# Kernel tuning notes

Measured on AMD Instinct MI355X. Metric: run time of the kernel, lower is better.

The kernel has to match this reference:

```python
import jax, jax.numpy as jnp
import numpy as np

N_NODES = 100000
N_EDGES = 800000
B = 4000            # number of pair subgraphs
GNN_IN = 428        # embed_dim(300) + 128 structural features
H = 64              # GIN hidden_channels
HID = 512           # PATH_DIM
EMB = 300           # numberbatch embedding dim
NUM_CLS = 151       # VG object classes
N_LAYERS = 3


def setup_inputs() -> dict:
    key = jax.random.key(0)
    ks = jax.random.split(key, 32)
    inp = {
        "pred_pairs": jax.random.randint(ks[0], (B, 2), 0, NUM_CLS, dtype=jnp.int32),
        "x": jax.random.normal(ks[1], (N_NODES, GNN_IN), dtype=jnp.float32),
        "edge_index": jax.random.randint(ks[2], (2, N_EDGES), 0, N_NODES, dtype=jnp.int32),
        "batch_ids": jnp.sort(jax.random.randint(ks[3], (N_NODES,), 0, B, dtype=jnp.int32)),
        "entity_embed": jax.random.normal(ks[4], (NUM_CLS, EMB), dtype=jnp.float32) * 0.05,
    }
    dins = [GNN_IN, H, H]
    for l in range(N_LAYERS):
        inp[f"w1_{l}"] = jax.random.normal(ks[5 + 4 * l], (dins[l], H), dtype=jnp.float32) * 0.05
        inp[f"b1_{l}"] = jnp.zeros((H,), dtype=jnp.float32)
        inp[f"w2_{l}"] = jax.random.normal(ks[6 + 4 * l], (H, H), dtype=jnp.float32) * 0.05
        inp[f"b2_{l}"] = jnp.zeros((H,), dtype=jnp.float32)
    inp["lin_w"] = jax.random.normal(ks[20], (H, HID), dtype=jnp.float32) * 0.05
    inp["lin_b"] = jnp.zeros((HID,), dtype=jnp.float32)
    inp["final_w"] = jax.random.normal(ks[21], (2 * EMB + HID, HID), dtype=jnp.float32) * 0.05
    inp["final_b"] = jnp.zeros((HID,), dtype=jnp.float32)
    return inp


def _gin_conv(h, src, dst, w1, b1, w2, b2):
    # GIN (eps=0): h_i' = MLP(h_i + sum_{j->i} h_j)
    agg = jax.ops.segment_sum(h[src], dst, num_segments=N_NODES)  # [N, d]
    z = h + agg
    z = jax.nn.relu(z @ w1 + b1)
    return jax.nn.relu(z @ w2 + b2)


def reference(pred_pairs, x, edge_index, batch_ids, entity_embed,
              w1_0, b1_0, w2_0, b2_0,
              w1_1, b1_1, w2_1, b2_1,
              w1_2, b1_2, w2_2, b2_2,
              lin_w, lin_b, final_w, final_b):
    src, dst = edge_index[0], edge_index[1]
    h = x
    for (w1, b1, w2, b2) in ((w1_0, b1_0, w2_0, b2_0),
                             (w1_1, b1_1, w2_1, b2_1),
                             (w1_2, b1_2, w2_2, b2_2)):
        h = _gin_conv(h, src, dst, w1, b1, w2, b2)
    # graph-level mean pooling over batch segments
    pooled = jax.ops.segment_sum(h, batch_ids, num_segments=B)              # [B, H]
    counts = jax.ops.segment_sum(jnp.ones((N_NODES,), h.dtype), batch_ids,
                                 num_segments=B)                            # [B]
    pooled = pooled / jnp.maximum(counts, 1.0)[:, None]
    emb = pooled @ lin_w + lin_b                                            # [B, HID]
    original = entity_embed[pred_pairs].reshape(B, 2 * EMB)                 # [B, 600]
    out = jnp.concatenate([emb, original], axis=1) @ final_w + final_b      # [B, HID]
    return out
```

## Files before the change

### kernel.cpp

```cpp
#include <hip/hip_runtime.h>
#include <hip/hip_bf16.h>

#define N_NODES 100000
#define N_EDGES 800000
#define BGRAPH  4000
#define GNN_IN  428
#define HDIM    64
#define HID     512
#define EMBD    300
#define AIN     1112
#define CAP     48
#define LSTR    72

typedef unsigned short u16;
typedef short bf16x8 __attribute__((ext_vector_type(8)));
typedef float f32x4  __attribute__((ext_vector_type(4)));

__device__ __forceinline__ u16 f2bf(float f) {
    union { float f; unsigned int u; } v; v.f = f;
    unsigned int r = v.u + 0x7FFFu + ((v.u >> 16) & 1u);
    return (u16)(r >> 16);
}
__device__ __forceinline__ float bf2f(u16 u) {
    union { unsigned int u; float f; } v; v.u = ((unsigned int)u) << 16;
    return v.f;
}

__global__ void k_prep_w0(const float* __restrict__ w, u16* __restrict__ w0T) {
    const int idx = blockIdx.x * 256 + threadIdx.x;
    if (idx >= 64 * 448) return;
    const int n = idx / 448, k = idx - n * 448;
    w0T[idx] = (k < GNN_IN) ? f2bf(w[k * 64 + n]) : (u16)0;
}
__global__ void k_prep_fw(const float* __restrict__ fw, u16* __restrict__ fwT) {
    const int idx = blockIdx.x * 256 + threadIdx.x;
    if (idx >= 512 * 1120) return;
    const int n = idx / 1120, k = idx - n * 1120;
    fwT[idx] = (k < AIN) ? f2bf(fw[(size_t)k * 512 + n]) : (u16)0;
}

__global__ __launch_bounds__(256) void k_gemm_xw(const float* __restrict__ x,
                                                 const u16* __restrict__ w0T,
                                                 u16* __restrict__ y) {
    __shared__ u16 xs[64 * 40];
    const int t = threadIdx.x;
    const int lane = t & 63, wave = t >> 6;
    const int q = lane >> 4, m = lane & 15;
    const int n0 = blockIdx.x * 64;

    f32x4 acc[4];
#pragma unroll
    for (int c = 0; c < 4; ++c) acc[c] = (f32x4){0.f, 0.f, 0.f, 0.f};

    for (int k0 = 0; k0 < 448; k0 += 32) {
#pragma unroll
        for (int h = 0; h < 2; ++h) {
            const int f = t + h * 256;
            const int row = f >> 3, fi = f & 7;
            const int gfi = (k0 >> 2) + fi;
            const int gr = n0 + row;
            float4 v = {0.f, 0.f, 0.f, 0.f};
            if (gr < N_NODES && gfi < 107)
                v = *reinterpret_cast<const float4*>(&x[(size_t)gr * GNN_IN + gfi * 4]);
            ushort4 b;
            b.x = f2bf(v.x); b.y = f2bf(v.y); b.z = f2bf(v.z); b.w = f2bf(v.w);
            *reinterpret_cast<ushort4*>(&xs[row * 40 + fi * 4]) = b;
        }
        __syncthreads();
        const bf16x8 a = *reinterpret_cast<const bf16x8*>(&xs[(wave * 16 + m) * 40 + q * 8]);
#pragma unroll
        for (int c = 0; c < 4; ++c) {
            const bf16x8 b = *reinterpret_cast<const bf16x8*>(&w0T[(c * 16 + m) * 448 + k0 + q * 8]);
            acc[c] = __builtin_amdgcn_mfma_f32_16x16x32_bf16(a, b, acc[c], 0, 0, 0);
        }
        __syncthreads();
    }
#pragma unroll
    for (int c = 0; c < 4; ++c)
#pragma unroll
        for (int r = 0; r < 4; ++r) {
            const int row = n0 + wave * 16 + q * 4 + r;
            if (row < N_NODES) y[(size_t)row * 64 + c * 16 + m] = f2bf(acc[c][r]);
        }
}

__global__ void k_fill(const int* __restrict__ ei, int* __restrict__ deg,
                       int* __restrict__ csr2) {
    const int e = blockIdx.x * blockDim.x + threadIdx.x;
    if (e >= N_EDGES) return;
    const int s = ei[e];
    const int d = ei[N_EDGES + e];
    const int slot = atomicAdd(&deg[d], 1);
    if (slot < CAP) csr2[d * CAP + slot] = s;
}

__global__ void k_counts(const int* __restrict__ bids, float* __restrict__ counts) {
    const int n = blockIdx.x * blockDim.x + threadIdx.x;
    if (n >= N_NODES) return;
    atomicAdd(&counts[bids[n]], 1.0f);
}

__device__ __forceinline__ float gather_bf(const u16* __restrict__ hin,
                                           const int* __restrict__ lst,
                                           int dg, int lane, float u) {
    const int4* l4 = reinterpret_cast<const int4*>(lst);
    for (int e = 0; e < dg; e += 8) {
        const int4 a = l4[(e >> 2) + 0];
        const int4 b = l4[(e >> 2) + 1];
        int id[8] = {a.x, a.y, a.z, a.w, b.x, b.y, b.z, b.w};
        float v[8];
#pragma unroll
        for (int i = 0; i < 8; ++i) {
            const int ok = (e + i < dg);
            const int idx = ok ? id[i] : id[0];
            v[i] = bf2f(hin[(size_t)idx * 64 + lane]) * (ok ? 1.f : 0.f);
        }
#pragma unroll
        for (int i = 0; i < 8; ++i) u += v[i];
    }
    return u;
}

__global__ __launch_bounds__(256) void k_gin0(const u16* __restrict__ y,
                                              const int* __restrict__ deg,
                                              const int* __restrict__ csr2,
                                              const float* __restrict__ b1,
                                              const float* __restrict__ w2,
                                              const float* __restrict__ b2,
                                              u16* __restrict__ hout) {
    __shared__ u16 zs[64 * LSTR];
    __shared__ u16 w2T[64 * LSTR];
    const int t = threadIdx.x;
    const int lane = t & 63, wave = t >> 6;
    const int q = lane >> 4, m = lane & 15;
    const int n0 = blockIdx.x * 64;
#pragma unroll
    for (int i = 0; i < 16; ++i) {
        const int idx = t + i * 256;
        const int k = idx >> 6, o = idx & 63;
        w2T[o * LSTR + k] = f2bf(w2[idx]);
    }
    const float b1v = b1[lane];
    for (int j = 0; j < 16; ++j) {
        const int n = n0 + wave * 16 + j;
        float u = 0.f;
        if (n < N_NODES) {
            u = bf2f(y[(size_t)n * 64 + lane]);
            const int dg = min(deg[n], CAP);
            u = gather_bf(y, &csr2[n * CAP], dg, lane, u);
            u = fmaxf(u + b1v, 0.f);
        }
        zs[(wave * 16 + j) * LSTR + lane] = f2bf(u);
    }
    __syncthreads();
    f32x4 acc[4];
#pragma unroll
    for (int c = 0; c < 4; ++c) acc[c] = (f32x4){0.f, 0.f, 0.f, 0.f};
    const bf16x8 a0 = *reinterpret_cast<const bf16x8*>(&zs[(wave * 16 + m) * LSTR + q * 8]);
    const bf16x8 a1 = *reinterpret_cast<const bf16x8*>(&zs[(wave * 16 + m) * LSTR + 32 + q * 8]);
#pragma unroll
    for (int c = 0; c < 4; ++c) {
        const bf16x8 bb0 = *reinterpret_cast<const bf16x8*>(&w2T[(c * 16 + m) * LSTR + q * 8]);
        const bf16x8 bb1 = *reinterpret_cast<const bf16x8*>(&w2T[(c * 16 + m) * LSTR + 32 + q * 8]);
        acc[c] = __builtin_amdgcn_mfma_f32_16x16x32_bf16(a0, bb0, acc[c], 0, 0, 0);
        acc[c] = __builtin_amdgcn_mfma_f32_16x16x32_bf16(a1, bb1, acc[c], 0, 0, 0);
    }
#pragma unroll
    for (int c = 0; c < 4; ++c) {
        const float bb = b2[c * 16 + m];
#pragma unroll
        for (int r = 0; r < 4; ++r) {
            const int n = n0 + wave * 16 + q * 4 + r;
            if (n < N_NODES) hout[(size_t)n * 64 + c * 16 + m] = f2bf(fmaxf(acc[c][r] + bb, 0.f));
        }
    }
}

__device__ __forceinline__ void gin_mfma2(const u16* __restrict__ hin,
                                          const int* __restrict__ deg,
                                          const int* __restrict__ csr2,
                                          const float* __restrict__ w1,
                                          const float* __restrict__ b1,
                                          const float* __restrict__ w2,
                                          const float* __restrict__ b2,
                                          u16* us, u16* zs, u16* w1T, u16* w2T,
                                          int n0, int t, f32x4 acc[4]) {
    const int lane = t & 63, wave = t >> 6;
    const int q = lane >> 4, m = lane & 15;
#pragma unroll
    for (int i = 0; i < 16; ++i) {
        const int idx = t + i * 256;
        const int k = idx >> 6, o = idx & 63;
        w1T[o * LSTR + k] = f2bf(w1[idx]);
        w2T[o * LSTR + k] = f2bf(w2[idx]);
    }
    for (int j = 0; j < 16; ++j) {
        const int n = n0 + wave * 16 + j;
        float u = 0.f;
        if (n < N_NODES) {
            u = bf2f(hin[(size_t)n * 64 + lane]);
            const int dg = min(deg[n], CAP);
            u = gather_bf(hin, &csr2[n * CAP], dg, lane, u);
        }
        us[(wave * 16 + j) * LSTR + lane] = f2bf(u);
    }
    __syncthreads();
    f32x4 z[4];
#pragma unroll
    for (int c = 0; c < 4; ++c) z[c] = (f32x4){0.f, 0.f, 0.f, 0.f};
    {
        const bf16x8 a0 = *reinterpret_cast<const bf16x8*>(&us[(wave * 16 + m) * LSTR + q * 8]);
        const bf16x8 a1 = *reinterpret_cast<const bf16x8*>(&us[(wave * 16 + m) * LSTR + 32 + q * 8]);
#pragma unroll
        for (int c = 0; c < 4; ++c) {
            const bf16x8 bb0 = *reinterpret_cast<const bf16x8*>(&w1T[(c * 16 + m) * LSTR + q * 8]);
            const bf16x8 bb1 = *reinterpret_cast<const bf16x8*>(&w1T[(c * 16 + m) * LSTR + 32 + q * 8]);
            z[c] = __builtin_amdgcn_mfma_f32_16x16x32_bf16(a0, bb0, z[c], 0, 0, 0);
            z[c] = __builtin_amdgcn_mfma_f32_16x16x32_bf16(a1, bb1, z[c], 0, 0, 0);
        }
    }
#pragma unroll
    for (int c = 0; c < 4; ++c) {
        const float bb = b1[c * 16 + m];
#pragma unroll
        for (int r = 0; r < 4; ++r)
            zs[(wave * 16 + q * 4 + r) * LSTR + c * 16 + m] = f2bf(fmaxf(z[c][r] + bb, 0.f));
    }
#pragma unroll
    for (int c = 0; c < 4; ++c) acc[c] = (f32x4){0.f, 0.f, 0.f, 0.f};
    {
        const bf16x8 a0 = *reinterpret_cast<const bf16x8*>(&zs[(wave * 16 + m) * LSTR + q * 8]);
        const bf16x8 a1 = *reinterpret_cast<const bf16x8*>(&zs[(wave * 16 + m) * LSTR + 32 + q * 8]);
#pragma unroll
        for (int c = 0; c < 4; ++c) {
            const bf16x8 bb0 = *reinterpret_cast<const bf16x8*>(&w2T[(c * 16 + m) * LSTR + q * 8]);
            const bf16x8 bb1 = *reinterpret_cast<const bf16x8*>(&w2T[(c * 16 + m) * LSTR + 32 + q * 8]);
            acc[c] = __builtin_amdgcn_mfma_f32_16x16x32_bf16(a0, bb0, acc[c], 0, 0, 0);
            acc[c] = __builtin_amdgcn_mfma_f32_16x16x32_bf16(a1, bb1, acc[c], 0, 0, 0);
        }
    }
}

__global__ __launch_bounds__(256) void k_gin(const u16* __restrict__ hin,
                                             const int* __restrict__ deg,
                                             const int* __restrict__ csr2,
                                             const float* __restrict__ w1,
                                             const float* __restrict__ b1,
                                             const float* __restrict__ w2,
                                             const float* __restrict__ b2,
                                             u16* __restrict__ hout) {
    __shared__ u16 us[64 * LSTR];
    __shared__ u16 zs[64 * LSTR];
    __shared__ u16 w1T[64 * LSTR];
    __shared__ u16 w2T[64 * LSTR];
    const int t = threadIdx.x;
    const int lane = t & 63, wave = t >> 6;
    const int q = lane >> 4, m = lane & 15;
    const int n0 = blockIdx.x * 64;
    f32x4 acc[4];
    gin_mfma2(hin, deg, csr2, w1, b1, w2, b2, us, zs, w1T, w2T, n0, t, acc);
#pragma unroll
    for (int c = 0; c < 4; ++c) {
        const float bb = b2[c * 16 + m];
#pragma unroll
        for (int r = 0; r < 4; ++r) {
            const int n = n0 + wave * 16 + q * 4 + r;
            if (n < N_NODES) hout[(size_t)n * 64 + c * 16 + m] = f2bf(fmaxf(acc[c][r] + bb, 0.f));
        }
    }
}

__global__ __launch_bounds__(256) void k_gin_pool(const u16* __restrict__ hin,
                                                  const int* __restrict__ deg,
                                                  const int* __restrict__ csr2,
                                                  const float* __restrict__ w1,
                                                  const float* __restrict__ b1,
                                                  const float* __restrict__ w2,
                                                  const float* __restrict__ b2,
                                                  const int* __restrict__ bids,
                                                  float* __restrict__ pooled) {
    __shared__ u16 us[64 * LSTR];
    __shared__ u16 zs[64 * LSTR];
    __shared__ u16 w1T[64 * LSTR];
    __shared__ u16 w2T[64 * LSTR];
    const int t = threadIdx.x;
    const int lane = t & 63, wave = t >> 6;
    const int q = lane >> 4, m = lane & 15;
    const int n0 = blockIdx.x * 64;
    f32x4 acc[4];
    gin_mfma2(hin, deg, csr2, w1, b1, w2, b2, us, zs, w1T, w2T, n0, t, acc);
#pragma unroll
    for (int c = 0; c < 4; ++c) {
        const float bb = b2[c * 16 + m];
#pragma unroll
        for (int r = 0; r < 4; ++r)
            us[(wave * 16 + q * 4 + r) * LSTR + c * 16 + m] = f2bf(fmaxf(acc[c][r] + bb, 0.f));
    }
    const int base = n0 + wave * 16;
    if (base < N_NODES) {
        float s = 0.f;
        int cur = bids[base];
        for (int j = 0; j < 16; ++j) {
            const int n = base + j;
            if (n >= N_NODES) break;
            const int b = bids[n];
            const float h = bf2f(us[(wave * 16 + j) * LSTR + lane]);
            if (b != cur) {
                atomicAdd(&pooled[cur * 64 + lane], s);
                cur = b; s = h;
            } else {
                s += h;
            }
        }
        atomicAdd(&pooled[cur * 64 + lane], s);
    }
}

__global__ __launch_bounds__(256) void k_emb(const float* __restrict__ pooled,
                                             const float* __restrict__ counts,
                                             const float* __restrict__ lw,
                                             const float* __restrict__ lb,
                                             u16* __restrict__ A) {
    __shared__ float prow[8][64];
    const int b0 = blockIdx.x * 8;
    const int t = threadIdx.x;
    const int lane = t & 63, wave = t >> 6;
    for (int i = 0; i < 2; ++i) {
        const int r = i * 4 + wave;
        const int b = b0 + r;
        const float c = fmaxf(counts[b], 1.0f);
        prow[r][lane] = pooled[b * 64 + lane] / c;
    }
    __syncthreads();
    for (int o = t; o < 512; o += 256) {
        float acc[8];
#pragma unroll
        for (int r = 0; r < 8; ++r) acc[r] = lb[o];
        for (int k = 0; k < 64; ++k) {
            const float wv = lw[k * 512 + o];
#pragma unroll
            for (int r = 0; r < 8; ++r) acc[r] += prow[r][k] * wv;
        }
#pragma unroll
        for (int r = 0; r < 8; ++r) A[(size_t)(b0 + r) * AIN + o] = f2bf(acc[r]);
    }
}

__global__ void k_orig(const int* __restrict__ pp, const float* __restrict__ ee,
                       u16* __restrict__ A) {
    const int idx = blockIdx.x * blockDim.x + threadIdx.x;
    if (idx >= BGRAPH * 600) return;
    const int b = idx / 600;
    const int j = idx - b * 600;
    const int which = (j >= 300) ? 1 : 0;
    const int cls = pp[b * 2 + which];
    A[(size_t)b * AIN + 512 + j] = f2bf(ee[cls * 300 + (j - which * 300)]);
}

__global__ __launch_bounds__(256) void k_final(const u16* __restrict__ A,
                                               const u16* __restrict__ fwT,
                                               const float* __restrict__ fb,
                                               float* __restrict__ out) {
    __shared__ u16 as[64 * 40];
    const int t = threadIdx.x;
    const int lane = t & 63, wave = t >> 6;
    const int q = lane >> 4, m = lane & 15;
    const int r0 = blockIdx.x * 64, c0 = blockIdx.y * 64;

    f32x4 acc[4];
#pragma unroll
    for (int c = 0; c < 4; ++c) acc[c] = (f32x4){0.f, 0.f, 0.f, 0.f};

    const int row = t >> 2, seg = t & 3;
    for (int k0 = 0; k0 < 1120; k0 += 32) {
        const int gr = r0 + row, gk = k0 + seg * 8;
        uint4 v = {0u, 0u, 0u, 0u};
        if (gr < BGRAPH && gk < AIN)
            v = *reinterpret_cast<const uint4*>(&A[(size_t)gr * AIN + gk]);
        *reinterpret_cast<uint4*>(&as[row * 40 + seg * 8]) = v;
        __syncthreads();
        const bf16x8 a = *reinterpret_cast<const bf16x8*>(&as[(wave * 16 + m) * 40 + q * 8]);
#pragma unroll
        for (int c = 0; c < 4; ++c) {
            const bf16x8 b = *reinterpret_cast<const bf16x8*>(&fwT[(size_t)(c0 + c * 16 + m) * 1120 + k0 + q * 8]);
            acc[c] = __builtin_amdgcn_mfma_f32_16x16x32_bf16(a, b, acc[c], 0, 0, 0);
        }
        __syncthreads();
    }
#pragma unroll
    for (int c = 0; c < 4; ++c) {
        const float bb = fb[c0 + c * 16 + m];
#pragma unroll
        for (int r = 0; r < 4; ++r) {
            const int rr = r0 + wave * 16 + q * 4 + r;
            if (rr < BGRAPH) out[(size_t)rr * 512 + c0 + c * 16 + m] = acc[c][r] + bb;
        }
    }
}

extern "C" void kernel_launch(void* const* d_in, const int* in_sizes, int n_in,
                              void* d_out, int out_size, void* d_ws, size_t ws_size,
                              hipStream_t stream) {
    const int*   pred_pairs = (const int*)d_in[0];
    const float* x          = (const float*)d_in[1];
    const int*   ei         = (const int*)d_in[2];
    const int*   bids       = (const int*)d_in[3];
    const float* ee         = (const float*)d_in[4];
    const float* w1_0 = (const float*)d_in[5];
    const float* b1_0 = (const float*)d_in[6];
    const float* w2_0 = (const float*)d_in[7];
    const float* b2_0 = (const float*)d_in[8];
    const float* w1_1 = (const float*)d_in[9];
    const float* b1_1 = (const float*)d_in[10];
    const float* w2_1 = (const float*)d_in[11];
    const float* b2_1 = (const float*)d_in[12];
    const float* w1_2 = (const float*)d_in[13];
    const float* b1_2 = (const float*)d_in[14];
    const float* w2_2 = (const float*)d_in[15];
    const float* b2_2 = (const float*)d_in[16];
    const float* lin_w   = (const float*)d_in[17];
    const float* lin_b   = (const float*)d_in[18];
    const float* final_w = (const float*)d_in[19];
    const float* final_b = (const float*)d_in[20];
    float* out = (float*)d_out;

    u16*   Y      = (u16*)d_ws;
    u16*   Hb     = Y + (size_t)N_NODES * 64;
    int*   csr2   = (int*)(Hb + (size_t)N_NODES * 64);
    int*   deg    = csr2 + (size_t)N_NODES * CAP;
    float* pooled = (float*)(deg + N_NODES);
    float* counts = pooled + (size_t)BGRAPH * 64;
    u16*   A      = (u16*)(counts + BGRAPH);
    u16*   w0T    = A + (size_t)BGRAPH * AIN;
    u16*   fwT    = w0T + 64 * 448;

    hipMemsetAsync(deg, 0, (size_t)(N_NODES + BGRAPH * 64 + BGRAPH) * sizeof(int), stream);

    k_prep_w0<<<(64 * 448 + 255) / 256, 256, 0, stream>>>(w1_0, w0T);
    k_prep_fw<<<(512 * 1120 + 255) / 256, 256, 0, stream>>>(final_w, fwT);
    k_fill<<<(N_EDGES + 255) / 256, 256, 0, stream>>>(ei, deg, csr2);
    k_counts<<<(N_NODES + 255) / 256, 256, 0, stream>>>(bids, counts);
    k_gemm_xw<<<(N_NODES + 63) / 64, 256, 0, stream>>>(x, w0T, Y);
    k_gin0<<<(N_NODES + 63) / 64, 256, 0, stream>>>(Y, deg, csr2, b1_0, w2_0, b2_0, Hb);
    k_gin<<<(N_NODES + 63) / 64, 256, 0, stream>>>(Hb, deg, csr2, w1_1, b1_1, w2_1, b2_1, Y);
    k_gin_pool<<<(N_NODES + 63) / 64, 256, 0, stream>>>(Y, deg, csr2, w1_2, b1_2, w2_2, b2_2, bids, pooled);
    k_emb<<<BGRAPH / 8, 256, 0, stream>>>(pooled, counts, lin_w, lin_b, A);
    k_orig<<<(BGRAPH * 600 + 255) / 256, 256, 0, stream>>>(pred_pairs, ee, A);
    k_final<<<dim3((BGRAPH + 63) / 64, 8), 256, 0, stream>>>(A, fwT, final_b, out);
}
```

Before: 616.0 us.

## Pretranspose GIN weights once, drop LDS staging and barriers, widen neighbor gather

The 64x64 GIN weights are now converted to transposed bf16 once by small prep kernels. The GIN kernels read them straight from global memory instead of every block rebuilding LDS copies, which cuts LDS use and per-block setup work. The first-layer GEMM now loads x rows directly into MFMA registers without an LDS tile and block barriers. The neighbor gather always issues 16 loads up front, with a rarely taken tail loop for higher degrees. Block barriers are removed because each wave only reads its own LDS rows, and launch bounds now ask for 4 blocks per CU to raise occupancy. The trade-offs are redundant loads of row 0 for low-degree nodes and uncoalesced x reads in the GEMM.

```diff
diff --git a/kernel.cpp b/kernel.cpp
--- a/kernel.cpp
+++ b/kernel.cpp
@@ -38,49 +38,48 @@
     const int n = idx / 1120, k = idx - n * 1120;
     fwT[idx] = (k < AIN) ? f2bf(fw[(size_t)k * 512 + n]) : (u16)0;
 }
+__global__ void k_prep_w64(const float* __restrict__ w, u16* __restrict__ wT) {
+    const int idx = blockIdx.x * 256 + threadIdx.x;
+    const int k = idx >> 6, o = idx & 63;
+    wT[o * 64 + k] = f2bf(w[idx]);
+}
 
 __global__ __launch_bounds__(256) void k_gemm_xw(const float* __restrict__ x,
                                                  const u16* __restrict__ w0T,
                                                  u16* __restrict__ y) {
-    __shared__ u16 xs[64 * 40];
     const int t = threadIdx.x;
     const int lane = t & 63, wave = t >> 6;
     const int q = lane >> 4, m = lane & 15;
     const int n0 = blockIdx.x * 64;
+    const int row = min(n0 + wave * 16 + m, N_NODES - 1);
+    const float* __restrict__ xr = &x[(size_t)row * GNN_IN];
 
     f32x4 acc[4];
 #pragma unroll
     for (int c = 0; c < 4; ++c) acc[c] = (f32x4){0.f, 0.f, 0.f, 0.f};
 
     for (int k0 = 0; k0 < 448; k0 += 32) {
-#pragma unroll
-        for (int h = 0; h < 2; ++h) {
-            const int f = t + h * 256;
-            const int row = f >> 3, fi = f & 7;
-            const int gfi = (k0 >> 2) + fi;
-            const int gr = n0 + row;
-            float4 v = {0.f, 0.f, 0.f, 0.f};
-            if (gr < N_NODES && gfi < 107)
-                v = *reinterpret_cast<const float4*>(&x[(size_t)gr * GNN_IN + gfi * 4]);
-            ushort4 b;
-            b.x = f2bf(v.x); b.y = f2bf(v.y); b.z = f2bf(v.z); b.w = f2bf(v.w);
-            *reinterpret_cast<ushort4*>(&xs[row * 40 + fi * 4]) = b;
-        }
-        __syncthreads();
-        const bf16x8 a = *reinterpret_cast<const bf16x8*>(&xs[(wave * 16 + m) * 40 + q * 8]);
+        const int ka = k0 + q * 8;
+        float4 va = {0.f, 0.f, 0.f, 0.f}, vb = {0.f, 0.f, 0.f, 0.f};
+        if (ka + 4 <= GNN_IN) va = *reinterpret_cast<const float4*>(xr + ka);
+        if (ka + 8 <= GNN_IN) vb = *reinterpret_cast<const float4*>(xr + ka + 4);
+        bf16x8 a;
+        a[0] = (short)f2bf(va.x); a[1] = (short)f2bf(va.y);
+        a[2] = (short)f2bf(va.z); a[3] = (short)f2bf(va.w);
+        a[4] = (short)f2bf(vb.x); a[5] = (short)f2bf(vb.y);
+        a[6] = (short)f2bf(vb.z); a[7] = (short)f2bf(vb.w);
 #pragma unroll
         for (int c = 0; c < 4; ++c) {
-            const bf16x8 b = *reinterpret_cast<const bf16x8*>(&w0T[(c * 16 + m) * 448 + k0 + q * 8]);
+            const bf16x8 b = *reinterpret_cast<const bf16x8*>(&w0T[(c * 16 + m) * 448 + ka]);
             acc[c] = __builtin_amdgcn_mfma_f32_16x16x32_bf16(a, b, acc[c], 0, 0, 0);
         }
-        __syncthreads();
     }
 #pragma unroll
     for (int c = 0; c < 4; ++c)
 #pragma unroll
         for (int r = 0; r < 4; ++r) {
-            const int row = n0 + wave * 16 + q * 4 + r;
-            if (row < N_NODES) y[(size_t)row * 64 + c * 16 + m] = f2bf(acc[c][r]);
+            const int rr = n0 + wave * 16 + q * 4 + r;
+            if (rr < N_NODES) y[(size_t)rr * 64 + c * 16 + m] = f2bf(acc[c][r]);
         }
 }
 
@@ -100,59 +99,60 @@
     atomicAdd(&counts[bids[n]], 1.0f);
 }
 
-__device__ __forceinline__ float gather_bf(const u16* __restrict__ hin,
+__device__ __forceinline__ float gather16p(const u16* __restrict__ hin,
                                            const int* __restrict__ lst,
                                            int dg, int lane, float u) {
     const int4* l4 = reinterpret_cast<const int4*>(lst);
-    for (int e = 0; e < dg; e += 8) {
-        const int4 a = l4[(e >> 2) + 0];
-        const int4 b = l4[(e >> 2) + 1];
-        int id[8] = {a.x, a.y, a.z, a.w, b.x, b.y, b.z, b.w};
-        float v[8];
-#pragma unroll
-        for (int i = 0; i < 8; ++i) {
-            const int ok = (e + i < dg);
-            const int idx = ok ? id[i] : id[0];
-            v[i] = bf2f(hin[(size_t)idx * 64 + lane]) * (ok ? 1.f : 0.f);
-        }
-#pragma unroll
-        for (int i = 0; i < 8; ++i) u += v[i];
+    const int4 ia = l4[0], ib = l4[1], ic = l4[2], id4 = l4[3];
+    int id[16] = {ia.x, ia.y, ia.z, ia.w, ib.x, ib.y, ib.z, ib.w,
+                  ic.x, ic.y, ic.z, ic.w, id4.x, id4.y, id4.z, id4.w};
+    float v[16];
+#pragma unroll
+    for (int i = 0; i < 16; ++i) {
+        const bool ok = (i < dg);
+        const int idx = ok ? id[i] : 0;
+        v[i] = bf2f(hin[(size_t)idx * 64 + lane]) * (ok ? 1.f : 0.f);
+    }
+#pragma unroll
+    for (int i = 0; i < 16; ++i) u += v[i];
+    if (__builtin_expect(dg > 16, 0)) {
+        for (int e = 16; e < dg; e += 8) {
+            const int4 a = l4[e >> 2];
+            const int4 b = l4[(e >> 2) + 1];
+            int id2[8] = {a.x, a.y, a.z, a.w, b.x, b.y, b.z, b.w};
+#pragma unroll
+            for (int i = 0; i < 8; ++i) {
+                const bool ok = (e + i < dg);
+                const int idx = ok ? id2[i] : 0;
+                u += bf2f(hin[(size_t)idx * 64 + lane]) * (ok ? 1.f : 0.f);
+            }
+        }
     }
     return u;
 }
 
-__global__ __launch_bounds__(256) void k_gin0(const u16* __restrict__ y,
-                                              const int* __restrict__ deg,
-                                              const int* __restrict__ csr2,
-                                              const float* __restrict__ b1,
-                                              const float* __restrict__ w2,
-                                              const float* __restrict__ b2,
-                                              u16* __restrict__ hout) {
+__global__ __launch_bounds__(256, 4) void k_gin0(const u16* __restrict__ y,
+                                                 const int* __restrict__ deg,
+                                                 const int* __restrict__ csr2,
+                                                 const float* __restrict__ b1,
+                                                 const u16* __restrict__ w2T,
+                                                 const float* __restrict__ b2,
+                                                 u16* __restrict__ hout) {
     __shared__ u16 zs[64 * LSTR];
-    __shared__ u16 w2T[64 * LSTR];
     const int t = threadIdx.x;
     const int lane = t & 63, wave = t >> 6;
     const int q = lane >> 4, m = lane & 15;
     const int n0 = blockIdx.x * 64;
-#pragma unroll
-    for (int i = 0; i < 16; ++i) {
-        const int idx = t + i * 256;
-        const int k = idx >> 6, o = idx & 63;
-        w2T[o * LSTR + k] = f2bf(w2[idx]);
-    }
+    const int base = n0 + wave * 16;
     const float b1v = b1[lane];
+#pragma unroll 2
     for (int j = 0; j < 16; ++j) {
-        const int n = n0 + wave * 16 + j;
-        float u = 0.f;
-        if (n < N_NODES) {
-            u = bf2f(y[(size_t)n * 64 + lane]);
-            const int dg = min(deg[n], CAP);
-            u = gather_bf(y, &csr2[n * CAP], dg, lane, u);
-            u = fmaxf(u + b1v, 0.f);
-        }
-        zs[(wave * 16 + j) * LSTR + lane] = f2bf(u);
-    }
-    __syncthreads();
+        const int n = min(base + j, N_NODES - 1);
+        const int dg = min(deg[n], CAP);
+        float u = bf2f(y[(size_t)n * 64 + lane]);
+        u = gather16p(y, &csr2[n * CAP], dg, lane, u);
+        zs[(wave * 16 + j) * LSTR + lane] = f2bf(fmaxf(u + b1v, 0.f));
+    }
     f32x4 acc[4];
 #pragma unroll
     for (int c = 0; c < 4; ++c) acc[c] = (f32x4){0.f, 0.f, 0.f, 0.f};
@@ -160,8 +160,8 @@
     const bf16x8 a1 = *reinterpret_cast<const bf16x8*>(&zs[(wave * 16 + m) * LSTR + 32 + q * 8]);
 #pragma unroll
     for (int c = 0; c < 4; ++c) {
-        const bf16x8 bb0 = *reinterpret_cast<const bf16x8*>(&w2T[(c * 16 + m) * LSTR + q * 8]);
-        const bf16x8 bb1 = *reinterpret_cast<const bf16x8*>(&w2T[(c * 16 + m) * LSTR + 32 + q * 8]);
+        const bf16x8 bb0 = *reinterpret_cast<const bf16x8*>(&w2T[(c * 16 + m) * 64 + q * 8]);
+        const bf16x8 bb1 = *reinterpret_cast<const bf16x8*>(&w2T[(c * 16 + m) * 64 + 32 + q * 8]);
         acc[c] = __builtin_amdgcn_mfma_f32_16x16x32_bf16(a0, bb0, acc[c], 0, 0, 0);
         acc[c] = __builtin_amdgcn_mfma_f32_16x16x32_bf16(a1, bb1, acc[c], 0, 0, 0);
     }
@@ -179,32 +179,22 @@
 __device__ __forceinline__ void gin_mfma2(const u16* __restrict__ hin,
                                           const int* __restrict__ deg,
                                           const int* __restrict__ csr2,
-                                          const float* __restrict__ w1,
+                                          const u16* __restrict__ w1T,
                                           const float* __restrict__ b1,
-                                          const float* __restrict__ w2,
-                                          const float* __restrict__ b2,
-                                          u16* us, u16* zs, u16* w1T, u16* w2T,
+                                          const u16* __restrict__ w2T,
+                                          u16* us, u16* zs,
                                           int n0, int t, f32x4 acc[4]) {
     const int lane = t & 63, wave = t >> 6;
     const int q = lane >> 4, m = lane & 15;
-#pragma unroll
-    for (int i = 0; i < 16; ++i) {
-        const int idx = t + i * 256;
-        const int k = idx >> 6, o = idx & 63;
-        w1T[o * LSTR + k] = f2bf(w1[idx]);
-        w2T[o * LSTR + k] = f2bf(w2[idx]);
-    }
+    const int base = n0 + wave * 16;
+#pragma unroll 2
     for (int j = 0; j < 16; ++j) {
-        const int n = n0 + wave * 16 + j;
-        float u = 0.f;
-        if (n < N_NODES) {
-            u = bf2f(hin[(size_t)n * 64 + lane]);
-            const int dg = min(deg[n], CAP);
-            u = gather_bf(hin, &csr2[n * CAP], dg, lane, u);
-        }
+        const int n = min(base + j, N_NODES - 1);
+        const int dg = min(deg[n], CAP);
+        float u = bf2f(hin[(size_t)n * 64 + lane]);
+        u = gather16p(hin, &csr2[n * CAP], dg, lane, u);
         us[(wave * 16 + j) * LSTR + lane] = f2bf(u);
     }
-    __syncthreads();
     f32x4 z[4];
 #pragma unroll
     for (int c = 0; c < 4; ++c) z[c] = (f32x4){0.f, 0.f, 0.f, 0.f};
@@ -213,8 +203,8 @@
         const bf16x8 a1 = *reinterpret_cast<const bf16x8*>(&us[(wave * 16 + m) * LSTR + 32 + q * 8]);
 #pragma unroll
         for (int c = 0; c < 4; ++c) {
-            const bf16x8 bb0 = *reinterpret_cast<const bf16x8*>(&w1T[(c * 16 + m) * LSTR + q * 8]);
-            const bf16x8 bb1 = *reinterpret_cast<const bf16x8*>(&w1T[(c * 16 + m) * LSTR + 32 + q * 8]);
+            const bf16x8 bb0 = *reinterpret_cast<const bf16x8*>(&w1T[(c * 16 + m) * 64 + q * 8]);
+            const bf16x8 bb1 = *reinterpret_cast<const bf16x8*>(&w1T[(c * 16 + m) * 64 + 32 + q * 8]);
             z[c] = __builtin_amdgcn_mfma_f32_16x16x32_bf16(a0, bb0, z[c], 0, 0, 0);
             z[c] = __builtin_amdgcn_mfma_f32_16x16x32_bf16(a1, bb1, z[c], 0, 0, 0);
         }
@@ -233,32 +223,30 @@
         const bf16x8 a1 = *reinterpret_cast<const bf16x8*>(&zs[(wave * 16 + m) * LSTR + 32 + q * 8]);
 #pragma unroll
         for (int c = 0; c < 4; ++c) {
-            const bf16x8 bb0 = *reinterpret_cast<const bf16x8*>(&w2T[(c * 16 + m) * LSTR + q * 8]);
-            const bf16x8 bb1 = *reinterpret_cast<const bf16x8*>(&w2T[(c * 16 + m) * LSTR + 32 + q * 8]);
+            const bf16x8 bb0 = *reinterpret_cast<const bf16x8*>(&w2T[(c * 16 + m) * 64 + q * 8]);
+            const bf16x8 bb1 = *reinterpret_cast<const bf16x8*>(&w2T[(c * 16 + m) * 64 + 32 + q * 8]);
             acc[c] = __builtin_amdgcn_mfma_f32_16x16x32_bf16(a0, bb0, acc[c], 0, 0, 0);
             acc[c] = __builtin_amdgcn_mfma_f32_16x16x32_bf16(a1, bb1, acc[c], 0, 0, 0);
         }
     }
 }
 
-__global__ __launch_bounds__(256) void k_gin(const u16* __restrict__ hin,
-                                             const int* __restrict__ deg,
-                                             const int* __restrict__ csr2,
-                                             const float* __restrict__ w1,
-                                             const float* __restrict__ b1,
-                                             const float* __restrict__ w2,
-                                             const float* __restrict__ b2,
-                                             u16* __restrict__ hout) {
+__global__ __launch_bounds__(256, 4) void k_gin(const u16* __restrict__ hin,
+                                                const int* __restrict__ deg,
+                                                const int* __restrict__ csr2,
+                                                const u16* __restrict__ w1T,
+                                                const float* __restrict__ b1,
+                                                const u16* __restrict__ w2T,
+                                                const float* __restrict__ b2,
+                                                u16* __restrict__ hout) {
     __shared__ u16 us[64 * LSTR];
     __shared__ u16 zs[64 * LSTR];
-    __shared__ u16 w1T[64 * LSTR];
-    __shared__ u16 w2T[64 * LSTR];
     const int t = threadIdx.x;
     const int lane = t & 63, wave = t >> 6;
     const int q = lane >> 4, m = lane & 15;
     const int n0 = blockIdx.x * 64;
     f32x4 acc[4];
-    gin_mfma2(hin, deg, csr2, w1, b1, w2, b2, us, zs, w1T, w2T, n0, t, acc);
+    gin_mfma2(hin, deg, csr2, w1T, b1, w2T, us, zs, n0, t, acc);
 #pragma unroll
     for (int c = 0; c < 4; ++c) {
         const float bb = b2[c * 16 + m];
@@ -270,25 +258,23 @@
     }
 }
 
-__global__ __launch_bounds__(256) void k_gin_pool(const u16* __restrict__ hin,
-                                                  const int* __restrict__ deg,
-                                                  const int* __restrict__ csr2,
-                                                  const float* __restrict__ w1,
-                                                  const float* __restrict__ b1,
-                                                  const float* __restrict__ w2,
-                                                  const float* __restrict__ b2,
-                                                  const int* __restrict__ bids,
-                                                  float* __restrict__ pooled) {
+__global__ __launch_bounds__(256, 4) void k_gin_pool(const u16* __restrict__ hin,
+                                                     const int* __restrict__ deg,
+                                                     const int* __restrict__ csr2,
+                                                     const u16* __restrict__ w1T,
+                                                     const float* __restrict__ b1,
+                                                     const u16* __restrict__ w2T,
+                                                     const float* __restrict__ b2,
+                                                     const int* __restrict__ bids,
+                                                     float* __restrict__ pooled) {
     __shared__ u16 us[64 * LSTR];
     __shared__ u16 zs[64 * LSTR];
-    __shared__ u16 w1T[64 * LSTR];
-    __shared__ u16 w2T[64 * LSTR];
     const int t = threadIdx.x;
     const int lane = t & 63, wave = t >> 6;
     const int q = lane >> 4, m = lane & 15;
     const int n0 = blockIdx.x * 64;
     f32x4 acc[4];
-    gin_mfma2(hin, deg, csr2, w1, b1, w2, b2, us, zs, w1T, w2T, n0, t, acc);
+    gin_mfma2(hin, deg, csr2, w1T, b1, w2T, us, zs, n0, t, acc);
 #pragma unroll
     for (int c = 0; c < 4; ++c) {
         const float bb = b2[c * 16 + m];
@@ -433,17 +419,27 @@
     u16*   A      = (u16*)(counts + BGRAPH);
     u16*   w0T    = A + (size_t)BGRAPH * AIN;
     u16*   fwT    = w0T + 64 * 448;
+    u16*   w2T0   = fwT + (size_t)512 * 1120;
+    u16*   w1T1   = w2T0 + 4096;
+    u16*   w2T1   = w1T1 + 4096;
+    u16*   w1T2   = w2T1 + 4096;
+    u16*   w2T2   = w1T2 + 4096;
 
     hipMemsetAsync(deg, 0, (size_t)(N_NODES + BGRAPH * 64 + BGRAPH) * sizeof(int), stream);
 
     k_prep_w0<<<(64 * 448 + 255) / 256, 256, 0, stream>>>(w1_0, w0T);
     k_prep_fw<<<(512 * 1120 + 255) / 256, 256, 0, stream>>>(final_w, fwT);
+    k_prep_w64<<<16, 256, 0, stream>>>(w2_0, w2T0);
+    k_prep_w64<<<16, 256, 0, stream>>>(w1_1, w1T1);
+    k_prep_w64<<<16, 256, 0, stream>>>(w2_1, w2T1);
+    k_prep_w64<<<16, 256, 0, stream>>>(w1_2, w1T2);
+    k_prep_w64<<<16, 256, 0, stream>>>(w2_2, w2T2);
     k_fill<<<(N_EDGES + 255) / 256, 256, 0, stream>>>(ei, deg, csr2);
     k_counts<<<(N_NODES + 255) / 256, 256, 0, stream>>>(bids, counts);
     k_gemm_xw<<<(N_NODES + 63) / 64, 256, 0, stream>>>(x, w0T, Y);
-    k_gin0<<<(N_NODES + 63) / 64, 256, 0, stream>>>(Y, deg, csr2, b1_0, w2_0, b2_0, Hb);
-    k_gin<<<(N_NODES + 63) / 64, 256, 0, stream>>>(Hb, deg, csr2, w1_1, b1_1, w2_1, b2_1, Y);
-    k_gin_pool<<<(N_NODES + 63) / 64, 256, 0, stream>>>(Y, deg, csr2, w1_2, b1_2, w2_2, b2_2, bids, pooled);
+    k_gin0<<<(N_NODES + 63) / 64, 256, 0, stream>>>(Y, deg, csr2, b1_0, w2T0, b2_0, Hb);
+    k_gin<<<(N_NODES + 63) / 64, 256, 0, stream>>>(Hb, deg, csr2, w1T1, b1_1, w2T1, b2_1, Y);
+    k_gin_pool<<<(N_NODES + 63) / 64, 256, 0, stream>>>(Y, deg, csr2, w1T2, b1_2, w2T2, b2_2, bids, pooled);
     k_emb<<<BGRAPH / 8, 256, 0, stream>>>(pooled, counts, lin_w, lin_b, A);
     k_orig<<<(BGRAPH * 600 + 255) / 256, 256, 0, stream>>>(pred_pairs, ee, A);
     k_final<<<dim3((BGRAPH + 63) / 64, 8), 256, 0, stream>>>(A, fwT, final_b, out);
```

Result: faster. 603.1 us (-2.1%).
